# Performance work log

Measured on AMD Instinct MI355X. Metric: run time of the kernel, lower is better.

Reference implementation:

```python
import jax, jax.numpy as jnp
import numpy as np

W_BITS = 4  # active precision (max of supported_bits)
EPS = 0.005  # clamp margin from the original module


def _dequant_kbit(qweight, lut, w_bits):
    """Bit-plane LUT dequant.
    qweight: [w_bits, O, I//32] int32, plane b holds bit b (MSB-first code) of each
    weight's k-bit index, 32 consecutive input positions per int32 word (LSB-first
    within a word). lut: [O, 2**w_bits]. Returns dense weight [O, I].
    """
    O = qweight.shape[1]
    shifts = jnp.arange(32, dtype=jnp.int32)                     # bit position within word
    bits = (qweight[:, :, :, None] >> shifts) & 1                # [w_bits, O, I//32, 32]
    plane_w = (1 << (w_bits - 1 - jnp.arange(w_bits, dtype=jnp.int32)))
    idx = (bits * plane_w[:, None, None, None]).sum(axis=0)      # [O, I//32, 32]
    idx = idx.reshape(O, -1)                                     # [O, I]
    return jnp.take_along_axis(lut, idx, axis=1)                 # [O, I]


def _csr_dense(rows, cols, vals, O, I):
    """Scatter CSR (indptr=rows) into a dense [O, I] matrix."""
    nnz = cols.shape[0]
    k = jnp.arange(nnz, dtype=rows.dtype)
    row_ids = jnp.searchsorted(rows, k, side='right') - 1        # CSR row of each nnz
    return jnp.zeros((O, I), dtype=vals.dtype).at[row_ids, cols].add(vals)


def setup_inputs() -> dict:
    key = jax.random.key(0)
    ks = jax.random.split(key, 7)
    B, S, I, O = 4, 2048, 4096, 4096
    NNZ = 65536
    x = jax.random.normal(ks[0], (B, S, I), dtype=jnp.float32)
    qweight = jax.random.randint(ks[1], (W_BITS, O, I // 32), 0, 2147483647, dtype=jnp.int32)
    lut = jax.random.normal(ks[2], (O, 2 ** W_BITS), dtype=jnp.float32) * 0.05
    rows = jnp.sort(jax.random.randint(ks[3], (O + 1,), 0, NNZ, dtype=jnp.int32))
    rows = rows.at[0].set(0).at[-1].set(NNZ)                     # valid CSR indptr
    cols = jax.random.randint(ks[4], (NNZ,), 0, I, dtype=jnp.int32)
    vals = jax.random.normal(ks[5], (NNZ,), dtype=jnp.float32) * 0.01
    bias = jax.random.normal(ks[6], (O,), dtype=jnp.float32) * 0.01
    return {"x": x, "qweight": qweight, "lut": lut, "rows": rows,
            "cols": cols, "vals": vals, "bias": bias}


def reference(x, qweight, lut, rows, cols, vals, bias):
    O = qweight.shape[1]
    I = x.shape[-1]
    weight = _dequant_kbit(qweight, lut, W_BITS)                 # [O, I]
    y = jnp.einsum('bsi,oi->bso', x, weight)                     # dense quantized GEMM
    w_sp = _csr_dense(rows, cols, vals, O, I)                    # sparse outlier weights
    y = y + jnp.einsum('bsi,oi->bso', x, w_sp)
    y = y + bias
    fmax = jnp.finfo(x.dtype).max * (1.0 - EPS)
    return jnp.clip(y, -fmax, fmax)
```

## Files before the change

kernel.cpp:

```cpp
#include <hip/hip_runtime.h>
#include <stdint.h>

#define Mdim 8192
#define Ndim 4096
#define Kdim 4096

#define BM 256
#define BN 256
#define BK 32
#define NT (Kdim / BK)

typedef float f32x4 __attribute__((ext_vector_type(4)));
typedef __bf16 bf16x8 __attribute__((ext_vector_type(8)));
typedef unsigned short ushort_t;

#define FMAXC 3.3858093490333422e+38f

__device__ __forceinline__ ushort_t f2bf(float f) {
    unsigned u = __float_as_uint(f);
    u += 0x7fffu + ((u >> 16) & 1u);
    return (ushort_t)(u >> 16);
}

__device__ __forceinline__ void gload_lds16(const void* g, void* l) {
    __builtin_amdgcn_global_load_lds(
        (const __attribute__((address_space(1))) uint32_t*)g,
        (__attribute__((address_space(3))) uint32_t*)(uint32_t)(uintptr_t)l,
        16, 0, 0);
}

__global__ __launch_bounds__(128) void dequant_kernel(
        const int* __restrict__ qw, const float* __restrict__ lut,
        const int* __restrict__ rows, const int* __restrict__ cols,
        const float* __restrict__ vals, ushort_t* __restrict__ w16) {
    __shared__ float wrow[128 * 33];
    __shared__ float slut[16];
    const int o = blockIdx.x;
    const int t = threadIdx.x;

    if (t < 16) slut[t] = lut[o * 16 + t];
    __syncthreads();

    const int q0 = qw[0 * Ndim * 128 + o * 128 + t];
    const int q1 = qw[1 * Ndim * 128 + o * 128 + t];
    const int q2 = qw[2 * Ndim * 128 + o * 128 + t];
    const int q3 = qw[3 * Ndim * 128 + o * 128 + t];
    float* dst = &wrow[t * 33];
#pragma unroll
    for (int j = 0; j < 32; ++j) {
        int idx = (((q0 >> j) & 1) << 3) | (((q1 >> j) & 1) << 2) |
                  (((q2 >> j) & 1) << 1) | ((q3 >> j) & 1);
        dst[j] = slut[idx];
    }
    __syncthreads();

    const int beg = rows[o], end = rows[o + 1];
    for (int k = beg + t; k < end; k += 128) {
        int c = cols[k];
        atomicAdd(&wrow[c + (c >> 5)], vals[k]);
    }
    __syncthreads();

    __align__(16) ushort_t tmp[32];
#pragma unroll
    for (int j = 0; j < 32; ++j) tmp[j] = f2bf(dst[j]);
    uint4* dstg = (uint4*)(w16 + (size_t)o * Kdim + t * 32);
    const uint4* srcg = (const uint4*)tmp;
#pragma unroll
    for (int j = 0; j < 4; ++j) dstg[j] = srcg[j];
}

__global__ __launch_bounds__(256) void convx_kernel(
        const float* __restrict__ x, ushort_t* __restrict__ y) {
    size_t i = ((size_t)blockIdx.x * 256 + threadIdx.x) * 8;
    float4 a = *(const float4*)(x + i);
    float4 b = *(const float4*)(x + i + 4);
    __align__(16) ushort_t r[8] = {f2bf(a.x), f2bf(a.y), f2bf(a.z), f2bf(a.w),
                                   f2bf(b.x), f2bf(b.y), f2bf(b.z), f2bf(b.w)};
    *(uint4*)(y + i) = *(const uint4*)r;
}

__global__ __launch_bounds__(512, 2) void gemm_kernel(
        const ushort_t* __restrict__ A, const ushort_t* __restrict__ Bw,
        const float* __restrict__ bias, float* __restrict__ C) {
    __shared__ __align__(16) char lds[131072];

    const int wgid = blockIdx.x;
    const int swz = (wgid & 7) * 64 + (wgid >> 3);
    const int bn = swz & 15, bm = swz >> 4;
    const int m0 = bm * BM, n0 = bn * BN;

    const int tid = threadIdx.x;
    const int lane = tid & 63, wid = tid >> 6;
    const int wr = wid >> 2, wc = wid & 3;
    const int fr = lane & 15, kg = lane >> 4;

    const int sline = tid >> 3;
    const int slot = (tid & 7) ^ (sline & 7);
    const int srow0 = (sline << 1) + (slot >> 2);
    const int skel = (slot & 3) * 8;
    const ushort_t* gA = A + (size_t)(m0 + srow0) * Kdim + skel;
    const ushort_t* gB = Bw + (size_t)(n0 + srow0) * Kdim + skel;

    const int offL = (fr >> 1) * 128 + (((((fr & 1) << 2) | kg) ^ (fr >> 1)) << 4);

    f32x4 acc[8][4];
#pragma unroll
    for (int i = 0; i < 8; ++i)
#pragma unroll
        for (int j = 0; j < 4; ++j) acc[i][j] = (f32x4){0.f, 0.f, 0.f, 0.f};

    const ushort_t* pA = gA;
    const ushort_t* pB = gB;

    auto stageA = [&](int bufd) {
        char* d = lds + bufd * 16384 + tid * 16;
        gload_lds16(pA, d);
        gload_lds16(pA + (size_t)128 * Kdim, d + 8192);
        pA += BK;
    };
    auto stageB = [&](int bufd) {
        char* d = lds + 65536 + bufd * 16384 + tid * 16;
        gload_lds16(pB, d);
        gload_lds16(pB + (size_t)128 * Kdim, d + 8192);
        pB += BK;
    };
    auto readAlo = [&](bf16x8 (&FA)[4], int buf) {
#pragma unroll
        for (int m = 0; m < 4; ++m)
            FA[m] = *(const bf16x8*)(lds + buf * 16384 + wr * 8192 + m * 1024 + offL);
    };
    auto readAhi = [&](bf16x8 (&FA)[4], int buf) {
#pragma unroll
        for (int m = 0; m < 4; ++m)
            FA[m] = *(const bf16x8*)(lds + buf * 16384 + wr * 8192 + (m + 4) * 1024 + offL);
    };
    auto readB = [&](bf16x8 (&FB)[4], int buf) {
#pragma unroll
        for (int n = 0; n < 4; ++n)
            FB[n] = *(const bf16x8*)(lds + 65536 + buf * 16384 + wc * 4096 + n * 1024 + offL);
    };
    auto mfmaHalf = [&](int mb, bf16x8 (&FA)[4], bf16x8 (&FB)[4]) {
        __builtin_amdgcn_s_setprio(1);
#pragma unroll
        for (int m = 0; m < 4; ++m)
#pragma unroll
            for (int n = 0; n < 4; ++n)
                acc[mb + m][n] = __builtin_amdgcn_mfma_f32_16x16x32_bf16(
                    FA[m], FB[n], acc[mb + m][n], 0, 0, 0);
        __builtin_amdgcn_s_setprio(0);
    };

    bf16x8 Ac[4], An[4], BA[4], BB[4];

    auto tileMain = [&](int t, bf16x8 (&Bc)[4], bf16x8 (&Bn)[4]) {
        const int bufR = t & 3, bufR1 = (t + 1) & 3, bufS = (t + 2) & 3;
        readAhi(An, bufR);
        stageA(bufS);
        asm volatile("s_waitcnt vmcnt(2)");
        __builtin_amdgcn_sched_barrier(0);
        __builtin_amdgcn_s_barrier();
        asm volatile("s_waitcnt lgkmcnt(4)");
        __builtin_amdgcn_sched_barrier(0);
        mfmaHalf(0, Ac, Bc);
        __builtin_amdgcn_s_barrier();
        readAlo(Ac, bufR1);
        readB(Bn, bufR1);
        stageB(bufS);
        __builtin_amdgcn_sched_barrier(0);
        __builtin_amdgcn_s_barrier();
        asm volatile("s_waitcnt lgkmcnt(8)");
        __builtin_amdgcn_sched_barrier(0);
        mfmaHalf(4, An, Bc);
        __builtin_amdgcn_s_barrier();
    };

    stageA(0); stageB(0);
    stageA(1); stageB(1);
    asm volatile("s_waitcnt vmcnt(4)");
    __builtin_amdgcn_sched_barrier(0);
    __builtin_amdgcn_s_barrier();
    readAlo(Ac, 0);
    readB(BA, 0);

#pragma unroll 1
    for (int t = 0; t < NT - 2; t += 2) {
        tileMain(t, BA, BB);
        tileMain(t + 1, BB, BA);
    }

    {
        const int bufR = (NT - 2) & 3, bufR1 = (NT - 1) & 3;
        readAhi(An, bufR);
        asm volatile("s_waitcnt vmcnt(0)");
        __builtin_amdgcn_sched_barrier(0);
        __builtin_amdgcn_s_barrier();
        asm volatile("s_waitcnt lgkmcnt(4)");
        __builtin_amdgcn_sched_barrier(0);
        mfmaHalf(0, Ac, BA);
        __builtin_amdgcn_s_barrier();
        readAlo(Ac, bufR1);
        readB(BB, bufR1);
        __builtin_amdgcn_sched_barrier(0);
        __builtin_amdgcn_s_barrier();
        asm volatile("s_waitcnt lgkmcnt(8)");
        __builtin_amdgcn_sched_barrier(0);
        mfmaHalf(4, An, BA);
        __builtin_amdgcn_s_barrier();
    }
    {
        const int bufR = (NT - 1) & 3;
        readAhi(An, bufR);
        asm volatile("s_waitcnt lgkmcnt(4)");
        __builtin_amdgcn_sched_barrier(0);
        mfmaHalf(0, Ac, BB);
        asm volatile("s_waitcnt lgkmcnt(0)");
        __builtin_amdgcn_sched_barrier(0);
        mfmaHalf(4, An, BB);
    }

    const int rg = lane >> 4;
#pragma unroll
    for (int nf = 0; nf < 4; ++nf) {
        const int col = n0 + wc * 64 + nf * 16 + fr;
        const float bv = bias[col];
#pragma unroll
        for (int mf = 0; mf < 8; ++mf) {
            const int row = m0 + wr * 128 + mf * 16 + rg * 4;
            float* outp = C + (size_t)row * Ndim + col;
#pragma unroll
            for (int j = 0; j < 4; ++j) {
                float v = acc[mf][nf][j] + bv;
                v = fminf(fmaxf(v, -FMAXC), FMAXC);
                outp[(size_t)j * Ndim] = v;
            }
        }
    }
}

extern "C" void kernel_launch(void* const* d_in, const int* in_sizes, int n_in,
                              void* d_out, int out_size, void* d_ws, size_t ws_size,
                              hipStream_t stream) {
    const float* x    = (const float*)d_in[0];
    const int*   qw   = (const int*)d_in[1];
    const float* lut  = (const float*)d_in[2];
    const int*   rows = (const int*)d_in[3];
    const int*   cols = (const int*)d_in[4];
    const float* vals = (const float*)d_in[5];
    const float* bias = (const float*)d_in[6];
    float* out = (float*)d_out;

    ushort_t* x16 = (ushort_t*)d_ws;
    ushort_t* w16 = x16 + (size_t)Mdim * Kdim;

    hipLaunchKernelGGL(dequant_kernel, dim3(Ndim), dim3(128), 0, stream,
                       qw, lut, rows, cols, vals, w16);
    hipLaunchKernelGGL(convx_kernel, dim3((Mdim * Kdim) / (256 * 8)), dim3(256), 0, stream,
                       x, x16);
    hipLaunchKernelGGL(gemm_kernel, dim3((Mdim / BM) * (Ndim / BN)), dim3(512), 0, stream,
                       x16, w16, bias, out);
}
```

Baseline: 302.9 us.

## Restructure GEMM main loop to double-buffered BK=64 with four-phase schedule

Replaces the 4-deep ring of BK=32 LDS buffers with two BK=64 buffers, each split into two K-halves. Every iteration runs four phases, each pairing an LDS fragment read and an async global-to-LDS stage with 16 MFMAs. The aim is fewer loop iterations and barriers per unit of K, and reuse of the B fragments across both M halves. In exchange each phase waits with lgkmcnt(0) instead of partial counts, and prefetch distance drops from two tiles to one, so load latency may be less well hidden.

```diff
diff --git a/kernel.cpp b/kernel.cpp
--- a/kernel.cpp
+++ b/kernel.cpp
@@ -7,8 +7,8 @@
 
 #define BM 256
 #define BN 256
-#define BK 32
-#define NT (Kdim / BK)
+#define BK 64
+#define NT2 (Kdim / BK)
 
 typedef float f32x4 __attribute__((ext_vector_type(4)));
 typedef __bf16 bf16x8 __attribute__((ext_vector_type(8)));
@@ -110,113 +110,109 @@
 #pragma unroll
         for (int j = 0; j < 4; ++j) acc[i][j] = (f32x4){0.f, 0.f, 0.f, 0.f};
 
-    const ushort_t* pA = gA;
-    const ushort_t* pB = gB;
-
-    auto stageA = [&](int bufd) {
-        char* d = lds + bufd * 16384 + tid * 16;
-        gload_lds16(pA, d);
-        gload_lds16(pA + (size_t)128 * Kdim, d + 8192);
-        pA += BK;
-    };
-    auto stageB = [&](int bufd) {
-        char* d = lds + 65536 + bufd * 16384 + tid * 16;
-        gload_lds16(pB, d);
-        gload_lds16(pB + (size_t)128 * Kdim, d + 8192);
-        pB += BK;
-    };
-    auto readAlo = [&](bf16x8 (&FA)[4], int buf) {
+    auto stageHalf = [&](const ushort_t* gsrc, int ldsOff, int koff) {
+        char* d = lds + ldsOff + tid * 16;
+        gload_lds16(gsrc + koff, d);
+        gload_lds16(gsrc + koff + (size_t)128 * Kdim, d + 8192);
+    };
+    auto readA4 = [&](bf16x8 (&F)[4], int base, int mh) {
 #pragma unroll
         for (int m = 0; m < 4; ++m)
-            FA[m] = *(const bf16x8*)(lds + buf * 16384 + wr * 8192 + m * 1024 + offL);
-    };
-    auto readAhi = [&](bf16x8 (&FA)[4], int buf) {
+            F[m] = *(const bf16x8*)(lds + base + wr * 8192 + (mh * 4 + m) * 1024 + offL);
+    };
+    auto readB4 = [&](bf16x8 (&F)[4], int base) {
+#pragma unroll
+        for (int n = 0; n < 4; ++n)
+            F[n] = *(const bf16x8*)(lds + base + wc * 4096 + n * 1024 + offL);
+    };
+    auto mfma16 = [&](int mh, bf16x8 (&FA)[4], bf16x8 (&FB)[4]) {
+        __builtin_amdgcn_s_setprio(1);
 #pragma unroll
         for (int m = 0; m < 4; ++m)
-            FA[m] = *(const bf16x8*)(lds + buf * 16384 + wr * 8192 + (m + 4) * 1024 + offL);
-    };
-    auto readB = [&](bf16x8 (&FB)[4], int buf) {
-#pragma unroll
-        for (int n = 0; n < 4; ++n)
-            FB[n] = *(const bf16x8*)(lds + 65536 + buf * 16384 + wc * 4096 + n * 1024 + offL);
-    };
-    auto mfmaHalf = [&](int mb, bf16x8 (&FA)[4], bf16x8 (&FB)[4]) {
-        __builtin_amdgcn_s_setprio(1);
-#pragma unroll
-        for (int m = 0; m < 4; ++m)
 #pragma unroll
             for (int n = 0; n < 4; ++n)
-                acc[mb + m][n] = __builtin_amdgcn_mfma_f32_16x16x32_bf16(
-                    FA[m], FB[n], acc[mb + m][n], 0, 0, 0);
+                acc[mh * 4 + m][n] = __builtin_amdgcn_mfma_f32_16x16x32_bf16(
+                    FA[m], FB[n], acc[mh * 4 + m][n], 0, 0, 0);
         __builtin_amdgcn_s_setprio(0);
     };
 
-    bf16x8 Ac[4], An[4], BA[4], BB[4];
-
-    auto tileMain = [&](int t, bf16x8 (&Bc)[4], bf16x8 (&Bn)[4]) {
-        const int bufR = t & 3, bufR1 = (t + 1) & 3, bufS = (t + 2) & 3;
-        readAhi(An, bufR);
-        stageA(bufS);
-        asm volatile("s_waitcnt vmcnt(2)");
-        __builtin_amdgcn_sched_barrier(0);
-        __builtin_amdgcn_s_barrier();
-        asm volatile("s_waitcnt lgkmcnt(4)");
-        __builtin_amdgcn_sched_barrier(0);
-        mfmaHalf(0, Ac, Bc);
-        __builtin_amdgcn_s_barrier();
-        readAlo(Ac, bufR1);
-        readB(Bn, bufR1);
-        stageB(bufS);
-        __builtin_amdgcn_sched_barrier(0);
-        __builtin_amdgcn_s_barrier();
-        asm volatile("s_waitcnt lgkmcnt(8)");
-        __builtin_amdgcn_sched_barrier(0);
-        mfmaHalf(4, An, Bc);
-        __builtin_amdgcn_s_barrier();
-    };
-
-    stageA(0); stageB(0);
-    stageA(1); stageB(1);
+    stageHalf(gA, 0, 0);
+    stageHalf(gB, 32768, 0);
+    stageHalf(gA, 16384, 32);
+    stageHalf(gB, 49152, 32);
     asm volatile("s_waitcnt vmcnt(4)");
     __builtin_amdgcn_sched_barrier(0);
     __builtin_amdgcn_s_barrier();
-    readAlo(Ac, 0);
-    readB(BA, 0);
 
 #pragma unroll 1
-    for (int t = 0; t < NT - 2; t += 2) {
-        tileMain(t, BA, BB);
-        tileMain(t + 1, BB, BA);
+    for (int t = 0; t < NT2 - 1; ++t) {
+        const int cb = (t & 1) * 65536, nb = ((t + 1) & 1) * 65536;
+        const int koff = (t + 1) * BK;
+        bf16x8 FA[4], FB0[4], FB1[4];
+
+        readA4(FA, cb, 0);
+        readB4(FB0, cb + 32768);
+        stageHalf(gA, nb, koff);
+        __builtin_amdgcn_s_barrier();
+        asm volatile("s_waitcnt lgkmcnt(0)");
+        __builtin_amdgcn_sched_barrier(0);
+        mfma16(0, FA, FB0);
+        __builtin_amdgcn_s_barrier();
+
+        readA4(FA, cb, 1);
+        stageHalf(gB, nb + 32768, koff);
+        __builtin_amdgcn_s_barrier();
+        asm volatile("s_waitcnt lgkmcnt(0)");
+        __builtin_amdgcn_sched_barrier(0);
+        mfma16(1, FA, FB0);
+        asm volatile("s_waitcnt vmcnt(4)");
+        __builtin_amdgcn_sched_barrier(0);
+        __builtin_amdgcn_s_barrier();
+
+        readA4(FA, cb + 16384, 0);
+        readB4(FB1, cb + 49152);
+        stageHalf(gA, nb + 16384, koff + 32);
+        __builtin_amdgcn_s_barrier();
+        asm volatile("s_waitcnt lgkmcnt(0)");
+        __builtin_amdgcn_sched_barrier(0);
+        mfma16(0, FA, FB1);
+        __builtin_amdgcn_s_barrier();
+
+        readA4(FA, cb + 16384, 1);
+        stageHalf(gB, nb + 49152, koff + 32);
+        __builtin_amdgcn_s_barrier();
+        asm volatile("s_waitcnt lgkmcnt(0)");
+        __builtin_amdgcn_sched_barrier(0);
+        mfma16(1, FA, FB1);
+        asm volatile("s_waitcnt vmcnt(4)");
+        __builtin_amdgcn_sched_barrier(0);
+        __builtin_amdgcn_s_barrier();
     }
 
     {
-        const int bufR = (NT - 2) & 3, bufR1 = (NT - 1) & 3;
-        readAhi(An, bufR);
+        const int cb = ((NT2 - 1) & 1) * 65536;
+        bf16x8 FA[4], FB0[4], FB1[4];
+        readA4(FA, cb, 0);
+        readB4(FB0, cb + 32768);
+        asm volatile("s_waitcnt lgkmcnt(0)");
+        __builtin_amdgcn_sched_barrier(0);
+        mfma16(0, FA, FB0);
+        readA4(FA, cb, 1);
+        asm volatile("s_waitcnt lgkmcnt(0)");
+        __builtin_amdgcn_sched_barrier(0);
+        mfma16(1, FA, FB0);
         asm volatile("s_waitcnt vmcnt(0)");
         __builtin_amdgcn_sched_barrier(0);
         __builtin_amdgcn_s_barrier();
-        asm volatile("s_waitcnt lgkmcnt(4)");
-        __builtin_amdgcn_sched_barrier(0);
-        mfmaHalf(0, Ac, BA);
-        __builtin_amdgcn_s_barrier();
-        readAlo(Ac, bufR1);
-        readB(BB, bufR1);
-        __builtin_amdgcn_sched_barrier(0);
-        __builtin_amdgcn_s_barrier();
-        asm volatile("s_waitcnt lgkmcnt(8)");
-        __builtin_amdgcn_sched_barrier(0);
-        mfmaHalf(4, An, BA);
-        __builtin_amdgcn_s_barrier();
-    }
-    {
-        const int bufR = (NT - 1) & 3;
-        readAhi(An, bufR);
-        asm volatile("s_waitcnt lgkmcnt(4)");
-        __builtin_amdgcn_sched_barrier(0);
-        mfmaHalf(0, Ac, BB);
-        asm volatile("s_waitcnt lgkmcnt(0)");
-        __builtin_amdgcn_sched_barrier(0);
-        mfmaHalf(4, An, BB);
+        readA4(FA, cb + 16384, 0);
+        readB4(FB1, cb + 49152);
+        asm volatile("s_waitcnt lgkmcnt(0)");
+        __builtin_amdgcn_sched_barrier(0);
+        mfma16(0, FA, FB1);
+        readA4(FA, cb + 16384, 1);
+        asm volatile("s_waitcnt lgkmcnt(0)");
+        __builtin_amdgcn_sched_barrier(0);
+        mfma16(1, FA, FB1);
     }
 
     const int rg = lane >> 4;
```

After: 290.7 us. 1.04x faster.
